# Kernel tuning notes

Hardware: AMD Instinct MI355X
Metric: run time of the kernel (lower is better)

Reference implementation:

```python
import jax, jax.numpy as jnp
import numpy as np

# Dimensions (match input_specs / init_kwargs)
T, B = 256, 128          # sequence length, batch
VOC, FLAGS = 256, 2      # vocabulary, speaker flags
IN_DIM = VOC + FLAGS     # one-hot char + flags
EMB = 512                # embedding size
N = 1024                 # LSTM nodes per layer
L = 2                    # num layers
H = L * N                # concat hidden size
WIN = 32                 # attention visibility window
OUT_EMB = 1024           # output embedding size


def setup_inputs() -> dict:
    key = jax.random.key(0)
    ks = jax.random.split(key, 8)
    s = jnp.float32(0.02)
    norm = lambda k, sh: jax.random.normal(k, sh, jnp.float32) * s
    return {
        "inp": jax.random.uniform(ks[0], (T, B, IN_DIM), jnp.float32),
        "emb_W": norm(ks[1], (IN_DIM, EMB)),
        "emb_b": jnp.zeros((EMB,), jnp.float32),
        # layer 0 sees concat([embedding, from_attention], h0): EMB+H+N -> 4N
        "M0": norm(ks[2], (EMB + H + N, 4 * N)),
        "B0": jnp.zeros((4 * N,), jnp.float32),
        # layer 1 sees concat(h0, h1): 2N -> 4N
        "M1": norm(ks[3], (2 * N, 4 * N)),
        "B1": jnp.zeros((4 * N,), jnp.float32),
        "Wg": norm(ks[4], (H, H)),          # output gates matrix
        "We": norm(ks[5], (H, OUT_EMB)),    # output embedding matrix
        "be": jnp.zeros((OUT_EMB,), jnp.float32),
        "Wo": norm(ks[6], (OUT_EMB, VOC)),  # output matrix
        "bo": jnp.zeros((VOC,), jnp.float32),
    }


def _lstm(bottom_up, h, c, M, b):
    # concat + matmul + bias, split to 3N sigmoid args and N tanh arg
    z = jnp.concatenate([bottom_up, h], axis=1) @ M + b
    gates = jax.nn.sigmoid(z[:, :3 * N])
    f, i, o = gates[:, :N], gates[:, N:2 * N], gates[:, 2 * N:]
    m = jnp.tanh(z[:, 3 * N:])
    c_new = c * f + m * i
    h_new = jnp.tanh(c_new) * o
    return h_new, c_new


def _forward(inp, emb_W, emb_b, M0, B0, M1, B1, Wg, We, be, Wo, bo):
    def step(carry, x):
        h0, c0, h1, c1, buf, from_att = carry
        e = x @ emb_W + emb_b                                  # _embed
        h0, c0 = _lstm(jnp.concatenate([e, from_att], 1), h0, c0, M0, B0)
        h1, c1 = _lstm(h0, h1, c1, M1, B1)
        hs = jnp.concatenate([h0, h1], 1)                      # [B, H]
        buf = jnp.concatenate([buf[1:], hs[None]], 0)
        # _renew_attention_vec
        scores = jax.nn.softmax(jnp.einsum('wbh,bh->bw', buf, hs), axis=1)
        from_att = jnp.einsum('wbh,bw->bh', buf, scores)       # [B, H]
        # _output_module: per-element sigmoid gates over concat hidden
        gated = jax.nn.sigmoid(hs @ Wg) * hs
        logits = jax.nn.relu(gated @ We + be) @ Wo + bo        # [B, VOC]
        return (h0, c0, h1, c1, buf, from_att), logits

    z = lambda *sh: jnp.zeros(sh, inp.dtype)
    carry0 = (z(B, N), z(B, N), z(B, N), z(B, N), z(WIN, B, H), z(B, H))
    _, logits = jax.lax.scan(step, carry0, inp)
    return logits  # [T, B, VOC]


def reference(inp, emb_W, emb_b, M0, B0, M1, B1, Wg, We, be, Wo, bo):
    return _forward(inp, emb_W, emb_b, M0, B0, M1, B1, Wg, We, be, Wo, bo)
```

## Files before the change

kernel.cpp:

```cpp
#include <hip/hip_runtime.h>
#include <hip/hip_bf16.h>
#include <math.h>

#define T_ 256
#define B_ 128
#define VOC_ 256
#define EMB_ 512
#define N_ 1024
#define H_ 2048
#define WIN_ 32
#define OUT_EMB_ 1024

typedef _Float16 half8 __attribute__((ext_vector_type(8)));
typedef float f32x4 __attribute__((ext_vector_type(4)));

__device__ __forceinline__ float sigmoidf_(float x) { return 1.f / (1.f + expf(-x)); }

__global__ __launch_bounds__(256)
void lstm_gemm(const _Float16* __restrict__ A0, int k0, int lda0,
               const _Float16* __restrict__ A1, int k1, int lda1,
               const _Float16* __restrict__ A2, int k2, int lda2,
               const _Float16* __restrict__ WT, int Ktot,
               const float* __restrict__ bias,
               float* __restrict__ c, _Float16* __restrict__ hH,
               _Float16* __restrict__ ringSlot, int ringHalf)
{
    __shared__ _Float16 As[2][64][72];
    __shared__ _Float16 Bs[2][32][72];

    const int tid = threadIdx.x;
    const int bn = blockIdx.x, bm = blockIdx.y;
    const int lane = tid & 63, wid = tid >> 6;
    const int wm = wid >> 1, wn = wid & 1;
    const int l15 = lane & 15, l4 = lane >> 4;

    const int arow = tid >> 2, akh = (tid & 3) * 16;
    const int brow = tid >> 3, bkh = (tid & 7) * 8;
    const _Float16* Bg = WT + (size_t)(bn * 32 + brow) * Ktot;

    const int NIT = Ktot >> 6;

    f32x4 acc[2];
    acc[0] = (f32x4){0.f, 0.f, 0.f, 0.f};
    acc[1] = (f32x4){0.f, 0.f, 0.f, 0.f};

    half8 pa0A, pa1A, pbA, pa0B, pa1B, pbB;

    auto issue = [&](int it, half8& r0, half8& r1, half8& rb) {
        const int kb = it * 64;
        const _Float16* Ag; int so, ld;
        if (kb < k0)           { Ag = A0; so = 0;       ld = lda0; }
        else if (kb < k0 + k1) { Ag = A1; so = k0;      ld = lda1; }
        else                   { Ag = A2; so = k0 + k1; ld = lda2; }
        const _Float16* ap = Ag + (size_t)(bm * 64 + arow) * ld + (kb - so);
        r0 = *(const half8*)(ap + akh);
        r1 = *(const half8*)(ap + akh + 8);
        rb = *(const half8*)(Bg + kb + bkh);
    };
    auto wlds = [&](int buf, half8 r0, half8 r1, half8 rb) {
        *(half8*)&As[buf][arow][akh]     = r0;
        *(half8*)&As[buf][arow][akh + 8] = r1;
        *(half8*)&Bs[buf][brow][bkh]     = rb;
    };
    auto comp = [&](int buf) {
        #pragma unroll
        for (int ks = 0; ks < 2; ++ks) {
            half8 a0 = *(half8*)&As[buf][wm * 32 + l15][ks * 32 + l4 * 8];
            half8 a1 = *(half8*)&As[buf][wm * 32 + 16 + l15][ks * 32 + l4 * 8];
            half8 b0 = *(half8*)&Bs[buf][wn * 16 + l15][ks * 32 + l4 * 8];
            acc[0] = __builtin_amdgcn_mfma_f32_16x16x32_f16(a0, b0, acc[0], 0, 0, 0);
            acc[1] = __builtin_amdgcn_mfma_f32_16x16x32_f16(a1, b0, acc[1], 0, 0, 0);
        }
    };

    issue(0, pa0A, pa1A, pbA);
    issue(1, pa0B, pa1B, pbB);
    wlds(0, pa0A, pa1A, pbA);
    __syncthreads();

    for (int it = 0; it < NIT; it += 2) {
        comp(0);
        if (it + 2 < NIT) issue(it + 2, pa0A, pa1A, pbA);
        __syncthreads();
        wlds(1, pa0B, pa1B, pbB);
        __syncthreads();
        comp(1);
        if (it + 3 < NIT) issue(it + 3, pa0B, pa1B, pbB);
        __syncthreads();
        if (it + 2 < NIT) wlds(0, pa0A, pa1A, pbA);
        __syncthreads();
    }

    const int cg = bn * 32 + wn * 16 + l15;
    const bool owner = (cg & 3) == 0;
    const int jglob = cg >> 2;
    float bf = 0.f, bi = 0.f, bo_ = 0.f, bm_ = 0.f;
    if (owner) {
        bf  = bias[jglob];
        bi  = bias[1024 + jglob];
        bo_ = bias[2048 + jglob];
        bm_ = bias[3072 + jglob];
    }
    #pragma unroll
    for (int fm = 0; fm < 2; ++fm) {
        const int rbase = bm * 64 + wm * 32 + fm * 16 + l4 * 4;
        #pragma unroll
        for (int jr = 0; jr < 4; ++jr) {
            float v  = acc[fm][jr];
            float v1 = __shfl_xor(v, 1);
            float v2 = __shfl_xor(v, 2);
            float v3 = __shfl_xor(v, 3);
            if (owner) {
                const int r = rbase + jr;
                float zf = v + bf, zi = v1 + bi, zo = v2 + bo_, zm = v3 + bm_;
                float f = sigmoidf_(zf), ii = sigmoidf_(zi), o = sigmoidf_(zo);
                float m = tanhf(zm);
                const int ci = r * 1024 + jglob;
                float cn = c[ci] * f + m * ii;
                float hn = tanhf(cn) * o;
                c[ci] = cn;
                hH[ci] = (_Float16)hn;
                ringSlot[r * 2048 + ringHalf + jglob] = (_Float16)hn;
            }
        }
    }
}

__global__ __launch_bounds__(256)
void gemm_h(const _Float16* __restrict__ A0, int k0, int lda0,
            const _Float16* __restrict__ BT, int ldb,
            int N, int Ktot, int M,
            float* __restrict__ Cf, _Float16* __restrict__ Ch,
            const float* __restrict__ bias, int mode)
{
    __shared__ _Float16 As[64][40];
    __shared__ _Float16 Bs[64][40];

    const int tid = threadIdx.x;
    const int bn = blockIdx.x, bm = blockIdx.y;
    const int lane = tid & 63, wid = tid >> 6;
    const int wm = wid >> 1, wn = wid & 1;
    const int l15 = lane & 15, l4 = lane >> 4;
    const int ar = tid >> 2, ak = (tid & 3) * 8;

    f32x4 acc[2][2];
    #pragma unroll
    for (int i = 0; i < 2; ++i)
        #pragma unroll
        for (int j = 0; j < 2; ++j) acc[i][j] = (f32x4){0.f, 0.f, 0.f, 0.f};

    for (int kb = 0; kb < Ktot; kb += 32) {
        *(half8*)&As[ar][ak] =
            *(const half8*)(A0 + (size_t)(bm * 64 + ar) * lda0 + (kb + ak));
        *(half8*)&Bs[ar][ak] =
            *(const half8*)(BT + (size_t)(bn * 64 + ar) * ldb + (kb + ak));
        __syncthreads();

        half8 a0 = *(half8*)&As[wm * 32 + l15][l4 * 8];
        half8 a1 = *(half8*)&As[wm * 32 + 16 + l15][l4 * 8];
        half8 b0 = *(half8*)&Bs[wn * 32 + l15][l4 * 8];
        half8 b1 = *(half8*)&Bs[wn * 32 + 16 + l15][l4 * 8];
        acc[0][0] = __builtin_amdgcn_mfma_f32_16x16x32_f16(a0, b0, acc[0][0], 0, 0, 0);
        acc[0][1] = __builtin_amdgcn_mfma_f32_16x16x32_f16(a0, b1, acc[0][1], 0, 0, 0);
        acc[1][0] = __builtin_amdgcn_mfma_f32_16x16x32_f16(a1, b0, acc[1][0], 0, 0, 0);
        acc[1][1] = __builtin_amdgcn_mfma_f32_16x16x32_f16(a1, b1, acc[1][1], 0, 0, 0);
        __syncthreads();
    }

    const int colb = bn * 64 + wn * 32 + l15;
    const int rowb = bm * 64 + wm * 32 + l4 * 4;
    #pragma unroll
    for (int fm = 0; fm < 2; ++fm)
        #pragma unroll
        for (int fn = 0; fn < 2; ++fn) {
            const int cgc = colb + fn * 16;
            const int rg = rowb + fm * 16;
            const float bv = bias ? bias[cgc] : 0.f;
            #pragma unroll
            for (int j = 0; j < 4; ++j) {
                float v = acc[fm][fn][j] + bv;
                if (mode == 1)      Cf[(size_t)(rg + j) * N + cgc] = v;
                else if (mode == 2) Ch[(size_t)(rg + j) * N + cgc] = (_Float16)fmaxf(v, 0.f);
                else                Ch[(size_t)(rg + j) * N + cgc] = (_Float16)v;
            }
        }
}

__global__ __launch_bounds__(256)
void attn_h(const _Float16* __restrict__ ring, int t, _Float16* __restrict__ faH)
{
    const int b = blockIdx.x, tid = threadIdx.x;
    __shared__ float hsl[2048];
    __shared__ float pl[32];

    const _Float16* hs = ring + ((size_t)(t & 31) * B_ + b) * 2048;
    {
        half8 v = *(const half8*)(hs + tid * 8);
        #pragma unroll
        for (int e = 0; e < 8; ++e) hsl[tid * 8 + e] = (float)v[e];
    }
    __syncthreads();

    const int wv = tid >> 6, lane = tid & 63;
    #pragma unroll
    for (int w8 = 0; w8 < 8; ++w8) {
        const int w = wv * 8 + w8;
        const int tw = t - 31 + w;
        float s = 0.f;
        if (tw >= 0) {
            const _Float16* br = ring + ((size_t)(tw & 31) * B_ + b) * 2048;
            #pragma unroll
            for (int p2 = 0; p2 < 4; ++p2) {
                half8 v = *(const half8*)(br + p2 * 512 + lane * 8);
                const float* hp = &hsl[p2 * 512 + lane * 8];
                #pragma unroll
                for (int e = 0; e < 8; ++e) s += (float)v[e] * hp[e];
            }
        }
        #pragma unroll
        for (int off = 32; off > 0; off >>= 1) s += __shfl_xor(s, off);
        if (lane == 0) pl[w] = s;
    }
    __syncthreads();

    if (tid < 64) {
        float v = (lane < 32) ? pl[lane] : -3.4e38f;
        float m = v;
        #pragma unroll
        for (int off = 32; off > 0; off >>= 1) m = fmaxf(m, __shfl_xor(m, off));
        float e = (lane < 32) ? expf(v - m) : 0.f;
        float ssum = e;
        #pragma unroll
        for (int off = 32; off > 0; off >>= 1) ssum += __shfl_xor(ssum, off);
        if (lane < 32) pl[lane] = e / ssum;
    }
    __syncthreads();

    float a[8] = {0.f, 0.f, 0.f, 0.f, 0.f, 0.f, 0.f, 0.f};
    for (int w = 0; w < 32; ++w) {
        const int tw = t - 31 + w;
        if (tw >= 0) {
            const float pw = pl[w];
            half8 v = *(const half8*)(ring + ((size_t)(tw & 31) * B_ + b) * 2048 + tid * 8);
            #pragma unroll
            for (int e = 0; e < 8; ++e) a[e] += pw * (float)v[e];
        }
    }
    #pragma unroll
    for (int e = 0; e < 8; ++e) faH[b * 2048 + tid * 8 + e] = (_Float16)a[e];
}

__global__ __launch_bounds__(256)
void gate_epi(const _Float16* __restrict__ Gh, const _Float16* __restrict__ hsC,
              _Float16* __restrict__ gatedH)
{
    int idx = blockIdx.x * 256 + threadIdx.x;
    gatedH[idx] = (_Float16)(sigmoidf_((float)Gh[idx]) * (float)hsC[idx]);
}

__global__ __launch_bounds__(256)
void transpose_cast(const float* __restrict__ W, int K, int N,
                    _Float16* __restrict__ WT, int Kp, int gperm)
{
    __shared__ float tile[32][33];
    const int tx = threadIdx.x & 31, ty8 = threadIdx.x >> 5;
    const int k0 = blockIdx.y * 32, n0 = blockIdx.x * 32;
    for (int yy = ty8; yy < 32; yy += 8) {
        int k = k0 + yy;
        tile[yy][tx] = (k < K) ? W[(size_t)k * N + n0 + tx] : 0.f;
    }
    __syncthreads();
    for (int yy = ty8; yy < 32; yy += 8) {
        int n = n0 + yy;
        int nd = gperm ? (((n & 1023) << 2) | (n >> 10)) : n;
        WT[(size_t)nd * Kp + k0 + tx] = (_Float16)tile[tx][yy];
    }
}

__global__ __launch_bounds__(256)
void cast_pad_inp(const float* __restrict__ inp, _Float16* __restrict__ inpH)
{
    int idx = blockIdx.x * 256 + threadIdx.x;
    int r = idx / 288, k = idx - r * 288;
    inpH[idx] = (k < 258) ? (_Float16)inp[(size_t)r * 258 + k] : (_Float16)0.f;
}

extern "C" void kernel_launch(void* const* d_in, const int* in_sizes, int n_in,
                              void* d_out, int out_size, void* d_ws, size_t ws_size,
                              hipStream_t stream)
{
    const float* inp  = (const float*)d_in[0];
    const float* embW = (const float*)d_in[1];
    const float* embB = (const float*)d_in[2];
    const float* M0   = (const float*)d_in[3];
    const float* B0   = (const float*)d_in[4];
    const float* M1   = (const float*)d_in[5];
    const float* B1   = (const float*)d_in[6];
    const float* Wg   = (const float*)d_in[7];
    const float* We   = (const float*)d_in[8];
    const float* be   = (const float*)d_in[9];
    const float* Wo   = (const float*)d_in[10];
    const float* bo   = (const float*)d_in[11];
    float* out = (float*)d_out;

    char* p = (char*)d_ws;
    float*    c0    = (float*)p;      p += 524288;
    float*    c1    = (float*)p;      p += 524288;
    _Float16* h0H   = (_Float16*)p;   p += 524288;
    _Float16* h1H   = (_Float16*)p;   p += 524288;
    _Float16* faH   = (_Float16*)p;   p += 524288;
    char* zero_base = (char*)c0; size_t zero_bytes = (size_t)(p - zero_base);
    _Float16* inpHc = (_Float16*)p;   p += (size_t)4096 * 288 * 2;
    _Float16* embWT = (_Float16*)p;   p += (size_t)512 * 288 * 2;
    _Float16* M0T   = (_Float16*)p;   p += (size_t)4096 * 3584 * 2;
    _Float16* M1T   = (_Float16*)p;   p += (size_t)4096 * 2048 * 2;
    _Float16* WgT   = (_Float16*)p;   p += (size_t)2048 * 2048 * 2;
    _Float16* WeT   = (_Float16*)p;   p += (size_t)1024 * 2048 * 2;
    _Float16* WoT   = (_Float16*)p;   p += (size_t)256 * 1024 * 2;
    _Float16* Ec    = (_Float16*)p;   p += (size_t)4096 * 512 * 2;
    _Float16* ring  = (_Float16*)p;   p += (size_t)32 * B_ * H_ * 2;
    _Float16* Gh    = (_Float16*)p;   p += (size_t)4096 * 2048 * 2;
    _Float16* gatedH= (_Float16*)p;   p += (size_t)4096 * 2048 * 2;
    _Float16* RH    = (_Float16*)p;   p += (size_t)4096 * 1024 * 2;
    if ((size_t)(p - (char*)d_ws) > ws_size) return;

    hipMemsetAsync(zero_base, 0, zero_bytes, stream);

    transpose_cast<<<dim3(16, 9),   256, 0, stream>>>(embW, 258, 512, embWT, 288, 0);
    transpose_cast<<<dim3(128, 112),256, 0, stream>>>(M0, 3584, 4096, M0T, 3584, 1);
    transpose_cast<<<dim3(128, 64), 256, 0, stream>>>(M1, 2048, 4096, M1T, 2048, 1);
    transpose_cast<<<dim3(64, 64),  256, 0, stream>>>(Wg, 2048, 2048, WgT, 2048, 0);
    transpose_cast<<<dim3(32, 64),  256, 0, stream>>>(We, 2048, 1024, WeT, 2048, 0);
    transpose_cast<<<dim3(8, 32),   256, 0, stream>>>(Wo, 1024, 256,  WoT, 1024, 0);

    for (int t = 0; t < T_; ++t) {
        if ((t & 31) == 0) {
            cast_pad_inp<<<4608, 256, 0, stream>>>(inp + (size_t)t * B_ * 258, inpHc);
            gemm_h<<<dim3(8, 64), 256, 0, stream>>>(
                inpHc, 288, 288, embWT, 288, 512, 288, 4096, nullptr, Ec, embB, 3);
        }
        const _Float16* Et = Ec + (size_t)(t & 31) * B_ * EMB_;
        _Float16* ringSlot = ring + (size_t)(t & 31) * B_ * H_;
        _Float16* h0p = h0H + (size_t)(t & 1) * 131072;
        _Float16* h0c = h0H + (size_t)((t + 1) & 1) * 131072;
        _Float16* h1p = h1H + (size_t)(t & 1) * 131072;
        _Float16* h1c = h1H + (size_t)((t + 1) & 1) * 131072;

        lstm_gemm<<<dim3(128, 2), 256, 0, stream>>>(
            Et, 512, 512, faH, 2048, 2048, h0p, 1024, 1024,
            M0T, 3584, B0, c0, h0c, ringSlot, 0);

        lstm_gemm<<<dim3(128, 2), 256, 0, stream>>>(
            h0c, 1024, 1024, h1p, 1024, 1024, nullptr, 0, 0,
            M1T, 2048, B1, c1, h1c, ringSlot, 1024);

        attn_h<<<128, 256, 0, stream>>>(ring, t, faH);

        if ((t & 31) == 31) {
            const int cch = t >> 5;
            gemm_h<<<dim3(32, 64), 256, 0, stream>>>(
                ring, 2048, 2048, WgT, 2048, 2048, 2048, 4096, nullptr, Gh, nullptr, 3);
            gate_epi<<<32768, 256, 0, stream>>>(Gh, ring, gatedH);
            gemm_h<<<dim3(16, 64), 256, 0, stream>>>(
                gatedH, 2048, 2048, WeT, 2048, 1024, 2048, 4096, nullptr, RH, be, 2);
            gemm_h<<<dim3(4, 64), 256, 0, stream>>>(
                RH, 1024, 1024, WoT, 1024, 256, 1024, 4096,
                out + (size_t)cch * 32 * B_ * VOC_, nullptr, bo, 1);
        }
    }
}
```

Measured before the change: 31.89 ms.

## Fuse per-step LSTM and attention kernels into persistent cooperative chunk kernel

Replaces the three per-timestep kernel launches (layer-0 LSTM, layer-1 LSTM, attention) with one cooperative kernel per 32-step chunk that loops over steps and uses grid-wide syncs between phases. This targets launch overhead and inter-kernel gaps in the serial recurrence. It relies on all 256 blocks being co-resident and reuses LDS tiles for attention scratch; grid.sync cost may offset the savings.

```diff
diff --git a/kernel.cpp b/kernel.cpp
--- a/kernel.cpp
+++ b/kernel.cpp
@@ -1,6 +1,9 @@
 #include <hip/hip_runtime.h>
 #include <hip/hip_bf16.h>
+#include <hip/hip_cooperative_groups.h>
 #include <math.h>
+
+namespace cg = cooperative_groups;
 
 #define T_ 256
 #define B_ 128
@@ -16,20 +19,18 @@
 
 __device__ __forceinline__ float sigmoidf_(float x) { return 1.f / (1.f + expf(-x)); }
 
-__global__ __launch_bounds__(256)
-void lstm_gemm(const _Float16* __restrict__ A0, int k0, int lda0,
-               const _Float16* __restrict__ A1, int k1, int lda1,
-               const _Float16* __restrict__ A2, int k2, int lda2,
-               const _Float16* __restrict__ WT, int Ktot,
-               const float* __restrict__ bias,
-               float* __restrict__ c, _Float16* __restrict__ hH,
-               _Float16* __restrict__ ringSlot, int ringHalf)
-{
-    __shared__ _Float16 As[2][64][72];
-    __shared__ _Float16 Bs[2][32][72];
-
+__device__ __forceinline__
+void lstm_gemm_body(_Float16 (*As)[64][72], _Float16 (*Bs)[32][72], int bid,
+                    const _Float16* __restrict__ A0, int k0, int lda0,
+                    const _Float16* __restrict__ A1, int k1, int lda1,
+                    const _Float16* __restrict__ A2, int k2, int lda2,
+                    const _Float16* __restrict__ WT, int Ktot,
+                    const float* __restrict__ bias,
+                    float* __restrict__ c, _Float16* __restrict__ hH,
+                    _Float16* __restrict__ ringSlot, int ringHalf)
+{
     const int tid = threadIdx.x;
-    const int bn = blockIdx.x, bm = blockIdx.y;
+    const int bn = bid & 127, bm = bid >> 7;
     const int lane = tid & 63, wid = tid >> 6;
     const int wm = wid >> 1, wn = wid & 1;
     const int l15 = lane & 15, l4 = lane >> 4;
@@ -91,9 +92,9 @@
         __syncthreads();
     }
 
-    const int cg = bn * 32 + wn * 16 + l15;
-    const bool owner = (cg & 3) == 0;
-    const int jglob = cg >> 2;
+    const int cgl = bn * 32 + wn * 16 + l15;
+    const bool owner = (cgl & 3) == 0;
+    const int jglob = cgl >> 2;
     float bf = 0.f, bi = 0.f, bo_ = 0.f, bm_ = 0.f;
     if (owner) {
         bf  = bias[jglob];
@@ -126,72 +127,12 @@
     }
 }
 
-__global__ __launch_bounds__(256)
-void gemm_h(const _Float16* __restrict__ A0, int k0, int lda0,
-            const _Float16* __restrict__ BT, int ldb,
-            int N, int Ktot, int M,
-            float* __restrict__ Cf, _Float16* __restrict__ Ch,
-            const float* __restrict__ bias, int mode)
-{
-    __shared__ _Float16 As[64][40];
-    __shared__ _Float16 Bs[64][40];
-
+__device__ __forceinline__
+void attn_body(float* hsl, float* pl, int b,
+               const _Float16* __restrict__ ring, int t,
+               _Float16* __restrict__ faH)
+{
     const int tid = threadIdx.x;
-    const int bn = blockIdx.x, bm = blockIdx.y;
-    const int lane = tid & 63, wid = tid >> 6;
-    const int wm = wid >> 1, wn = wid & 1;
-    const int l15 = lane & 15, l4 = lane >> 4;
-    const int ar = tid >> 2, ak = (tid & 3) * 8;
-
-    f32x4 acc[2][2];
-    #pragma unroll
-    for (int i = 0; i < 2; ++i)
-        #pragma unroll
-        for (int j = 0; j < 2; ++j) acc[i][j] = (f32x4){0.f, 0.f, 0.f, 0.f};
-
-    for (int kb = 0; kb < Ktot; kb += 32) {
-        *(half8*)&As[ar][ak] =
-            *(const half8*)(A0 + (size_t)(bm * 64 + ar) * lda0 + (kb + ak));
-        *(half8*)&Bs[ar][ak] =
-            *(const half8*)(BT + (size_t)(bn * 64 + ar) * ldb + (kb + ak));
-        __syncthreads();
-
-        half8 a0 = *(half8*)&As[wm * 32 + l15][l4 * 8];
-        half8 a1 = *(half8*)&As[wm * 32 + 16 + l15][l4 * 8];
-        half8 b0 = *(half8*)&Bs[wn * 32 + l15][l4 * 8];
-        half8 b1 = *(half8*)&Bs[wn * 32 + 16 + l15][l4 * 8];
-        acc[0][0] = __builtin_amdgcn_mfma_f32_16x16x32_f16(a0, b0, acc[0][0], 0, 0, 0);
-        acc[0][1] = __builtin_amdgcn_mfma_f32_16x16x32_f16(a0, b1, acc[0][1], 0, 0, 0);
-        acc[1][0] = __builtin_amdgcn_mfma_f32_16x16x32_f16(a1, b0, acc[1][0], 0, 0, 0);
-        acc[1][1] = __builtin_amdgcn_mfma_f32_16x16x32_f16(a1, b1, acc[1][1], 0, 0, 0);
-        __syncthreads();
-    }
-
-    const int colb = bn * 64 + wn * 32 + l15;
-    const int rowb = bm * 64 + wm * 32 + l4 * 4;
-    #pragma unroll
-    for (int fm = 0; fm < 2; ++fm)
-        #pragma unroll
-        for (int fn = 0; fn < 2; ++fn) {
-            const int cgc = colb + fn * 16;
-            const int rg = rowb + fm * 16;
-            const float bv = bias ? bias[cgc] : 0.f;
-            #pragma unroll
-            for (int j = 0; j < 4; ++j) {
-                float v = acc[fm][fn][j] + bv;
-                if (mode == 1)      Cf[(size_t)(rg + j) * N + cgc] = v;
-                else if (mode == 2) Ch[(size_t)(rg + j) * N + cgc] = (_Float16)fmaxf(v, 0.f);
-                else                Ch[(size_t)(rg + j) * N + cgc] = (_Float16)v;
-            }
-        }
-}
-
-__global__ __launch_bounds__(256)
-void attn_h(const _Float16* __restrict__ ring, int t, _Float16* __restrict__ faH)
-{
-    const int b = blockIdx.x, tid = threadIdx.x;
-    __shared__ float hsl[2048];
-    __shared__ float pl[32];
 
     const _Float16* hs = ring + ((size_t)(t & 31) * B_ + b) * 2048;
     {
@@ -248,6 +189,115 @@
     }
     #pragma unroll
     for (int e = 0; e < 8; ++e) faH[b * 2048 + tid * 8 + e] = (_Float16)a[e];
+}
+
+struct ChunkArgs {
+    const _Float16* Ec;
+    const _Float16* M0T;
+    const _Float16* M1T;
+    const float* B0;
+    const float* B1;
+    float* c0;
+    float* c1;
+    _Float16* h0H;
+    _Float16* h1H;
+    _Float16* faH;
+    _Float16* ring;
+    int t0;
+};
+
+__global__ __launch_bounds__(256)
+void recurrence_chunk(ChunkArgs a)
+{
+    __shared__ _Float16 As[2][64][72];
+    __shared__ _Float16 Bs[2][32][72];
+    cg::grid_group grid = cg::this_grid();
+    const int bid = blockIdx.x;
+
+    for (int s = 0; s < 32; ++s) {
+        const int t = a.t0 + s;
+        const _Float16* Et = a.Ec + (size_t)s * B_ * EMB_;
+        _Float16* ringSlot = a.ring + (size_t)(t & 31) * B_ * H_;
+        _Float16* h0p = a.h0H + (size_t)(t & 1) * 131072;
+        _Float16* h0c = a.h0H + (size_t)((t + 1) & 1) * 131072;
+        _Float16* h1p = a.h1H + (size_t)(t & 1) * 131072;
+        _Float16* h1c = a.h1H + (size_t)((t + 1) & 1) * 131072;
+
+        lstm_gemm_body(As, Bs, bid, Et, 512, 512, a.faH, 2048, 2048,
+                       h0p, 1024, 1024, a.M0T, 3584, a.B0, a.c0, h0c,
+                       ringSlot, 0);
+        grid.sync();
+
+        lstm_gemm_body(As, Bs, bid, h0c, 1024, 1024, h1p, 1024, 1024,
+                       nullptr, 0, 0, a.M1T, 2048, a.B1, a.c1, h1c,
+                       ringSlot, 1024);
+        grid.sync();
+
+        if (bid < 128)
+            attn_body((float*)&As[0][0][0], (float*)&Bs[0][0][0], bid,
+                      a.ring, t, a.faH);
+        grid.sync();
+    }
+}
+
+__global__ __launch_bounds__(256)
+void gemm_h(const _Float16* __restrict__ A0, int k0, int lda0,
+            const _Float16* __restrict__ BT, int ldb,
+            int N, int Ktot, int M,
+            float* __restrict__ Cf, _Float16* __restrict__ Ch,
+            const float* __restrict__ bias, int mode)
+{
+    __shared__ _Float16 As[64][40];
+    __shared__ _Float16 Bs[64][40];
+
+    const int tid = threadIdx.x;
+    const int bn = blockIdx.x, bm = blockIdx.y;
+    const int lane = tid & 63, wid = tid >> 6;
+    const int wm = wid >> 1, wn = wid & 1;
+    const int l15 = lane & 15, l4 = lane >> 4;
+    const int ar = tid >> 2, ak = (tid & 3) * 8;
+
+    f32x4 acc[2][2];
+    #pragma unroll
+    for (int i = 0; i < 2; ++i)
+        #pragma unroll
+        for (int j = 0; j < 2; ++j) acc[i][j] = (f32x4){0.f, 0.f, 0.f, 0.f};
+
+    for (int kb = 0; kb < Ktot; kb += 32) {
+        *(half8*)&As[ar][ak] =
+            *(const half8*)(A0 + (size_t)(bm * 64 + ar) * lda0 + (kb + ak));
+        *(half8*)&Bs[ar][ak] =
+            *(const half8*)(BT + (size_t)(bn * 64 + ar) * ldb + (kb + ak));
+        __syncthreads();
+
+        half8 a0 = *(half8*)&As[wm * 32 + l15][l4 * 8];
+        half8 a1 = *(half8*)&As[wm * 32 + 16 + l15][l4 * 8];
+        half8 b0 = *(half8*)&Bs[wn * 32 + l15][l4 * 8];
+        half8 b1 = *(half8*)&Bs[wn * 32 + 16 + l15][l4 * 8];
+        acc[0][0] = __builtin_amdgcn_mfma_f32_16x16x32_f16(a0, b0, acc[0][0], 0, 0, 0);
+        acc[0][1] = __builtin_amdgcn_mfma_f32_16x16x32_f16(a0, b1, acc[0][1], 0, 0, 0);
+        acc[1][0] = __builtin_amdgcn_mfma_f32_16x16x32_f16(a1, b0, acc[1][0], 0, 0, 0);
+        acc[1][1] = __builtin_amdgcn_mfma_f32_16x16x32_f16(a1, b1, acc[1][1], 0, 0, 0);
+        __syncthreads();
+    }
+
+    const int colb = bn * 64 + wn * 32 + l15;
+    const int rowb = bm * 64 + wm * 32 + l4 * 4;
+    #pragma unroll
+    for (int fm = 0; fm < 2; ++fm)
+        #pragma unroll
+        for (int fn = 0; fn < 2; ++fn) {
+            const int cgc = colb + fn * 16;
+            const int rg = rowb + fm * 16;
+            const float bv = bias ? bias[cgc] : 0.f;
+            #pragma unroll
+            for (int j = 0; j < 4; ++j) {
+                float v = acc[fm][fn][j] + bv;
+                if (mode == 1)      Cf[(size_t)(rg + j) * N + cgc] = v;
+                else if (mode == 2) Ch[(size_t)(rg + j) * N + cgc] = (_Float16)fmaxf(v, 0.f);
+                else                Ch[(size_t)(rg + j) * N + cgc] = (_Float16)v;
+            }
+        }
 }
 
 __global__ __launch_bounds__(256)
@@ -333,39 +383,28 @@
     transpose_cast<<<dim3(32, 64),  256, 0, stream>>>(We, 2048, 1024, WeT, 2048, 0);
     transpose_cast<<<dim3(8, 32),   256, 0, stream>>>(Wo, 1024, 256,  WoT, 1024, 0);
 
-    for (int t = 0; t < T_; ++t) {
-        if ((t & 31) == 0) {
-            cast_pad_inp<<<4608, 256, 0, stream>>>(inp + (size_t)t * B_ * 258, inpHc);
-            gemm_h<<<dim3(8, 64), 256, 0, stream>>>(
-                inpHc, 288, 288, embWT, 288, 512, 288, 4096, nullptr, Ec, embB, 3);
-        }
-        const _Float16* Et = Ec + (size_t)(t & 31) * B_ * EMB_;
-        _Float16* ringSlot = ring + (size_t)(t & 31) * B_ * H_;
-        _Float16* h0p = h0H + (size_t)(t & 1) * 131072;
-        _Float16* h0c = h0H + (size_t)((t + 1) & 1) * 131072;
-        _Float16* h1p = h1H + (size_t)(t & 1) * 131072;
-        _Float16* h1c = h1H + (size_t)((t + 1) & 1) * 131072;
-
-        lstm_gemm<<<dim3(128, 2), 256, 0, stream>>>(
-            Et, 512, 512, faH, 2048, 2048, h0p, 1024, 1024,
-            M0T, 3584, B0, c0, h0c, ringSlot, 0);
-
-        lstm_gemm<<<dim3(128, 2), 256, 0, stream>>>(
-            h0c, 1024, 1024, h1p, 1024, 1024, nullptr, 0, 0,
-            M1T, 2048, B1, c1, h1c, ringSlot, 1024);
-
-        attn_h<<<128, 256, 0, stream>>>(ring, t, faH);
-
-        if ((t & 31) == 31) {
-            const int cch = t >> 5;
-            gemm_h<<<dim3(32, 64), 256, 0, stream>>>(
-                ring, 2048, 2048, WgT, 2048, 2048, 2048, 4096, nullptr, Gh, nullptr, 3);
-            gate_epi<<<32768, 256, 0, stream>>>(Gh, ring, gatedH);
-            gemm_h<<<dim3(16, 64), 256, 0, stream>>>(
-                gatedH, 2048, 2048, WeT, 2048, 1024, 2048, 4096, nullptr, RH, be, 2);
-            gemm_h<<<dim3(4, 64), 256, 0, stream>>>(
-                RH, 1024, 1024, WoT, 1024, 256, 1024, 4096,
-                out + (size_t)cch * 32 * B_ * VOC_, nullptr, bo, 1);
-        }
-    }
-}
+    for (int cch = 0; cch < 8; ++cch) {
+        const int t0 = cch * 32;
+
+        cast_pad_inp<<<4608, 256, 0, stream>>>(inp + (size_t)t0 * B_ * 258, inpHc);
+        gemm_h<<<dim3(8, 64), 256, 0, stream>>>(
+            inpHc, 288, 288, embWT, 288, 512, 288, 4096, nullptr, Ec, embB, 3);
+
+        ChunkArgs ca;
+        ca.Ec = Ec; ca.M0T = M0T; ca.M1T = M1T; ca.B0 = B0; ca.B1 = B1;
+        ca.c0 = c0; ca.c1 = c1; ca.h0H = h0H; ca.h1H = h1H;
+        ca.faH = faH; ca.ring = ring; ca.t0 = t0;
+        void* kp[] = { &ca };
+        hipLaunchCooperativeKernel(recurrence_chunk, dim3(256), dim3(256),
+                                   kp, 0, stream);
+
+        gemm_h<<<dim3(32, 64), 256, 0, stream>>>(
+            ring, 2048, 2048, WgT, 2048, 2048, 2048, 4096, nullptr, Gh, nullptr, 3);
+        gate_epi<<<32768, 256, 0, stream>>>(Gh, ring, gatedH);
+        gemm_h<<<dim3(16, 64), 256, 0, stream>>>(
+            gatedH, 2048, 2048, WeT, 2048, 1024, 2048, 4096, nullptr, RH, be, 2);
+        gemm_h<<<dim3(4, 64), 256, 0, stream>>>(
+            RH, 1024, 1024, WoT, 1024, 256, 1024, 4096,
+            out + (size_t)cch * 32 * B_ * VOC_, nullptr, bo, 1);
+    }
+}
```

New measurement: 56.08 ms. 75.8% more time.
